# Kernel tuning notes

Hardware: AMD Instinct MI355X
Metric: run time of the kernel (lower is better)

## Reference

```python
import jax, jax.numpy as jnp
import numpy as np

B = 4096
IND = 512
OUTD = 512
DEG = 2
P = 2  # dim_treat
KNOTS = [[0.33, 0.66], [0.33, 0.66]]
D = DEG + 1 + len(KNOTS[0])  # 5 basis functions per treatment dim


def setup_inputs() -> dict:
    key = jax.random.key(0)
    k1, k2, k3 = jax.random.split(key, 3)
    x = jax.random.uniform(k1, (B, P + IND), dtype=jnp.float32)  # treat dims in [0,1]
    weight = jax.random.uniform(k2, (IND, OUTD, D ** P), dtype=jnp.float32)  # torch.rand init
    bias = jax.random.uniform(k3, (OUTD, D ** P), dtype=jnp.float32)
    return {"x": x, "weight": weight, "bias": bias}


def _truncated_power_basis(x_treat):
    # x_treat: [B, P] -> basis: [B, P, D]
    knots = jnp.asarray(KNOTS, dtype=x_treat.dtype)  # [P, n_knots]
    # polynomial part: 1, x, x^2, ... x^DEG
    pows = jnp.stack([x_treat ** i for i in range(DEG + 1)], axis=-1)  # [B, P, DEG+1]
    # truncated part: relu(x - knot)^DEG  (DEG > 1 branch of original code)
    trunc = jax.nn.relu(x_treat[:, :, None] - knots[None, :, :]) ** DEG  # [B, P, n_knots]
    return jnp.concatenate([pows, trunc], axis=-1)


def reference(x, weight, bias):
    x_treat = x[:, :P]          # [B, P]
    x_feature = x[:, P:]        # [B, IND]
    basis = _truncated_power_basis(x_treat)  # [B, P, D]
    # Kronecker product across the two treatment dims: outer product, flattened
    kb = jnp.einsum('bi,bj->bij', basis[:, 0, :], basis[:, 1, :]).reshape(x.shape[0], D * P * 0 + D * D)  # [B, D^2]
    # fused: (weight^T @ x_feature) contracted with the per-sample basis coefficients
    out = jnp.einsum('bi,iod,bd->bo', x_feature, weight, kb)  # [B, OUTD]
    out = out + kb @ bias.T      # bias also varies with treatment basis
    out = jax.nn.relu(out)       # act='relu'
    # islastlayer=0: re-attach treatment dims
    return jnp.concatenate([x_treat, out], axis=1)  # [B, P + OUTD]
```

## Files before the change

### kernel.cpp

```cpp
#include <hip/hip_runtime.h>
#include <hip/hip_bf16.h>
#include <string.h>

#define NB    4096
#define IND_  512
#define OUTD_ 512
#define XCOLS 514
#define ND    25
#define KTOT  12800
#define NSPL  4

#define WT_DS   262144
#define WT_BIAS 6553600

#define BM 32
#define BN 128

#define PWI 64
#define PWO 4
#define PWC (PWO * ND)
#define T8P 112

typedef float  f32x4  __attribute__((ext_vector_type(4)));
typedef int    i32x4  __attribute__((ext_vector_type(4)));
typedef int    i32x8  __attribute__((ext_vector_type(8)));
typedef unsigned short u16x4 __attribute__((ext_vector_type(4)));
typedef unsigned int   u32x2 __attribute__((ext_vector_type(2)));

__device__ __forceinline__ unsigned short f2bf(float f) {
  unsigned int x = __float_as_uint(f);
  return (unsigned short)((x + 0x7fffu + ((x >> 16) & 1u)) >> 16);
}

__device__ __forceinline__ float bf2f(unsigned short u) {
  return __uint_as_float(((unsigned int)u) << 16);
}

__device__ __forceinline__ unsigned int pk_bf16(float a, float b) {
  return (unsigned int)f2bf(a) | ((unsigned int)f2bf(b) << 16);
}

__device__ __forceinline__ unsigned char f2fp8(float v) {
  if (v < 0.015625f) {
    return (unsigned char)__float2int_rn(v * 512.0f);
  }
  unsigned int u = __float_as_uint(v);
  u += 0x7ffffu + ((u >> 20) & 1u);
  int e = (int)(u >> 23) - 127 + 7;
  unsigned int m = (u >> 20) & 7u;
  return (unsigned char)((e << 3) | m);
}

__device__ __forceinline__ float basis_f(float t, int j) {
  switch (j) {
    case 0: return 1.0f;
    case 1: return t;
    case 2: return t * t;
    case 3: { float r = t - 0.33f; r = r > 0.0f ? r : 0.0f; return r * r; }
    default:{ float r = t - 0.66f; r = r > 0.0f ? r : 0.0f; return r * r; }
  }
}

__global__ __launch_bounds__(256) void prep_all_kernel(
    const float* __restrict__ x, const float* __restrict__ W,
    const float* __restrict__ bias, unsigned char* __restrict__ Xf8,
    float* __restrict__ kbDT, unsigned char* __restrict__ kbT8,
    unsigned char* __restrict__ Wt, float* __restrict__ out)
{
  __shared__ unsigned char tile8[PWI * T8P];
  const int bid = blockIdx.x;
  const int tid = threadIdx.x;

  if (bid < 512) {
    const int lane = tid & 63;
    #pragma unroll
    for (int rr = 0; rr < 2; ++rr) {
      const int b = bid * 8 + (tid >> 6) * 2 + rr;
      const float* xr = x + (size_t)b * XCOLS;
      const float* fp = xr + 2 + lane * 8;
      float2 a0 = *(const float2*)(fp + 0);
      float2 a1 = *(const float2*)(fp + 2);
      float2 a2 = *(const float2*)(fp + 4);
      float2 a3 = *(const float2*)(fp + 6);
      float xf[8] = {a0.x, a0.y, a1.x, a1.y, a2.x, a2.y, a3.x, a3.y};
      u32x2 pk;
      pk[0] = (unsigned int)f2fp8(xf[0]) | ((unsigned int)f2fp8(xf[1]) << 8) |
              ((unsigned int)f2fp8(xf[2]) << 16) | ((unsigned int)f2fp8(xf[3]) << 24);
      pk[1] = (unsigned int)f2fp8(xf[4]) | ((unsigned int)f2fp8(xf[5]) << 8) |
              ((unsigned int)f2fp8(xf[6]) << 16) | ((unsigned int)f2fp8(xf[7]) << 24);
      *reinterpret_cast<u32x2*>(Xf8 + (size_t)b * IND_ + lane * 8) = pk;

      float t0 = xr[0], t1 = xr[1];
      if (lane < 2) out[(size_t)b * XCOLS + lane] = (lane == 0) ? t0 : t1;
      {
        int d1 = lane / 5, d2 = lane - d1 * 5;
        float kvd = basis_f(t0, d1) * basis_f(t1, d2);
        float kvn = 0.0f;
        if (lane < 24) {
          int e1 = (lane + 1) / 5, e2 = (lane + 1) - e1 * 5;
          kvn = basis_f(t0, e1) * basis_f(t1, e2);
        }
        if (lane < ND) {
          int bt = b >> 7, bl = b & 15, nf = (b >> 4) & 7;
          kbDT[(((size_t)lane * 32 + bt) * 16 + bl) * 8 + nf] = kvd - kvn;
        }
      }
      {
        int ta = 2 * lane, tb = 2 * lane + 1;
        unsigned char ba = 0, bb = 0;
        if (ta < ND) { int d1 = ta / 5, d2 = ta - d1 * 5;
                       ba = f2fp8(basis_f(t0, d1) * basis_f(t1, d2)); }
        if (tb < ND) { int d1 = tb / 5, d2 = tb - d1 * 5;
                       bb = f2fp8(basis_f(t0, d1) * basis_f(t1, d2)); }
        *(unsigned short*)(kbT8 + (size_t)b * 128 + 2 * lane) =
            (unsigned short)ba | ((unsigned short)bb << 8);
      }
    }
  } else {
    const int pw = bid - 512;
    const int i0 = (pw & 7) * PWI;
    const int o0 = (pw >> 3) * PWO;

    for (int t = tid; t < PWI * (PWC / 4); t += 256) {
      int il = t / (PWC / 4);
      int c4 = t - il * (PWC / 4);
      float4 v = *(const float4*)(W + ((size_t)(i0 + il) * OUTD_ + o0) * ND + c4 * 4);
      unsigned int pk = (unsigned int)f2fp8(v.x) | ((unsigned int)f2fp8(v.y) << 8) |
                        ((unsigned int)f2fp8(v.z) << 16) | ((unsigned int)f2fp8(v.w) << 24);
      *(unsigned int*)&tile8[il * T8P + c4 * 4] = pk;
    }
    __syncthreads();

    for (int g = tid; g < PWC * (PWI / 8); g += 256) {
      int c  = g >> 3;
      int ig = g & 7;
      int d  = c % 25;
      int o_l = c / 25;
      unsigned long long v = 0;
      #pragma unroll
      for (int jj = 0; jj < 8; ++jj)
        v |= (unsigned long long)tile8[(ig * 8 + jj) * T8P + c] << (8 * jj);
      int o  = o0 + o_l;
      int ib = i0 + ig * 8;
      int iw = ib >> 7;
      int wb = ib & 127;
      size_t dest = (((size_t)d * 32 + (o >> 4)) * 4 + iw) * 2048
                  + (size_t)(((wb >> 5) * 16 + (o & 15)) * 32 + (wb & 31));
      *reinterpret_cast<unsigned long long*>(Wt + dest) = v;
    }

    if ((pw & 7) == 0) {
      int o = o0 + (tid >> 6);
      int p = tid & 63;
      int ta = 2 * p, tb = 2 * p + 1;
      unsigned char ba = (ta < ND) ? f2fp8(bias[o * ND + ta]) : (unsigned char)0;
      unsigned char bb = (tb < ND) ? f2fp8(bias[o * ND + tb]) : (unsigned char)0;
      size_t dest = WT_BIAS + (size_t)(o >> 4) * 2048
                  + (size_t)(((ta >> 5) * 16 + (o & 15)) * 32 + (ta & 31));
      *(unsigned short*)(Wt + dest) =
          (unsigned short)ba | ((unsigned short)bb << 8);
    }
  }
}

__global__ __launch_bounds__(256, 3) void gemm_mx_kernel(
    const unsigned char* __restrict__ Wt, const unsigned char* __restrict__ Xf8,
    const float* __restrict__ kbDT, const unsigned char* __restrict__ kbT8,
    unsigned short* __restrict__ Pb)
{
  const int tid  = threadIdx.x;
  const int lane = tid & 63;
  const int w    = tid >> 6;
  const int l15  = lane & 15;
  const int quad = lane >> 4;

  const int id  = blockIdx.x;
  const int ox  = ((id & 7) << 1) | ((id >> 3) & 1);
  const int iw  = (id >> 4) & 3;
  const int by  = id >> 6;

  const int o0 = ox * BM;
  const int b0 = by * BN;
  const bool tail = (iw == 3);

  const int og = ox * 2 + (w >> 1);
  const int bh = w & 1;

  auto load8 = [](const unsigned char* p) -> i32x8 {
    i32x4 lo = *reinterpret_cast<const i32x4*>(p);
    i32x4 hi = *reinterpret_cast<const i32x4*>(p + 16);
    i32x8 v;
    v[0] = lo[0]; v[1] = lo[1]; v[2] = lo[2]; v[3] = lo[3];
    v[4] = hi[0]; v[5] = hi[1]; v[6] = hi[2]; v[7] = hi[3];
    return v;
  };

  i32x8 bfr[4];
  #pragma unroll
  for (int nf = 0; nf < 4; ++nf)
    bfr[nf] = load8(Xf8 + (size_t)(b0 + bh * 64 + nf * 16 + l15) * IND_
                        + iw * 128 + quad * 32);

  const unsigned char* aP =
      Wt + ((size_t)og * 4 + iw) * 2048 + lane * 32;

  const float* dP = kbDT + (((size_t)by * 16 + l15) * 8) + bh * 4;

  f32x4 acc[4], fin[4];
  #pragma unroll
  for (int nf = 0; nf < 4; ++nf) { acc[nf] = (f32x4)0.0f; fin[nf] = (f32x4)0.0f; }

  auto mfma_flush = [&](const i32x8& a, const f32x4& q) {
    #pragma unroll
    for (int nf = 0; nf < 4; ++nf)
      acc[nf] = __builtin_amdgcn_mfma_scale_f32_16x16x128_f8f6f4(
          a, bfr[nf], acc[nf], 0, 0, 0, 0x7f7f7f7f, 0, 0x7f7f7f7f);
    #pragma unroll
    for (int nf = 0; nf < 4; ++nf)
      #pragma unroll
      for (int r = 0; r < 4; ++r)
        fin[nf][r] += q[nf] * acc[nf][r];
  };

  i32x8 a0 = load8(aP);
  i32x8 a1 = load8(aP + WT_DS);
  i32x8 a2;
  f32x4 qA = *reinterpret_cast<const f32x4*>(dP);
  f32x4 qB, qC;

  for (int pass = 0; pass < 8; ++pass) {
    a2 = load8(aP + 2 * WT_DS);
    qB = *reinterpret_cast<const f32x4*>(dP + 4096);
    mfma_flush(a0, qA);

    a0 = load8(aP + 3 * WT_DS);
    qC = *reinterpret_cast<const f32x4*>(dP + 8192);
    mfma_flush(a1, qB);

    a1 = load8(aP + 4 * WT_DS);
    qA = *reinterpret_cast<const f32x4*>(dP + 12288);
    mfma_flush(a2, qC);

    aP += 3 * WT_DS;
    dP += 12288;
  }

  if (tail) a1 = load8(Wt + WT_BIAS + (size_t)og * 2048 + lane * 32);
  mfma_flush(a0, qA);

  if (tail) {
    i32x8 bft[4];
    #pragma unroll
    for (int nf = 0; nf < 4; ++nf)
      bft[nf] = load8(kbT8 + (size_t)(b0 + bh * 64 + nf * 16 + l15) * 128
                           + quad * 32);
    #pragma unroll
    for (int nf = 0; nf < 4; ++nf)
      fin[nf] = __builtin_amdgcn_mfma_scale_f32_16x16x128_f8f6f4(
          a1, bft[nf], fin[nf], 0, 0, 0, 0x7f7f7f7f, 0, 0x7f7f7f7f);
  }

  unsigned short* Pz = Pb + (size_t)iw * NB * OUTD_;
  #pragma unroll
  for (int nf = 0; nf < 4; ++nf) {
    int bg = b0 + bh * 64 + nf * 16 + l15;
    int oo = o0 + (w >> 1) * 16 + quad * 4;
    u32x2 pk;
    pk[0] = pk_bf16(fin[nf][0], fin[nf][1]);
    pk[1] = pk_bf16(fin[nf][2], fin[nf][3]);
    *reinterpret_cast<u32x2*>(&Pz[(size_t)bg * OUTD_ + oo]) = pk;
  }
}

__global__ __launch_bounds__(256) void epilogue_kernel(
    const unsigned short* __restrict__ Pb, float* __restrict__ out)
{
  const int idx = (blockIdx.x * 256 + threadIdx.x) * 4;
  const int b = idx >> 9;
  const int o = idx & 511;
  const size_t ps = (size_t)NB * OUTD_;
  float s[4] = {0.0f, 0.0f, 0.0f, 0.0f};
  #pragma unroll
  for (int z = 0; z < NSPL; ++z) {
    u16x4 v = *reinterpret_cast<const u16x4*>(&Pb[z * ps + idx]);
    #pragma unroll
    for (int e = 0; e < 4; ++e) s[e] += bf2f(v[e]);
  }
  float* op = out + (size_t)b * XCOLS + 2 + o;
  float2 lo, hi;
  lo.x = s[0] > 0.0f ? s[0] : 0.0f;
  lo.y = s[1] > 0.0f ? s[1] : 0.0f;
  hi.x = s[2] > 0.0f ? s[2] : 0.0f;
  hi.y = s[3] > 0.0f ? s[3] : 0.0f;
  *(float2*)op = lo;
  *(float2*)(op + 2) = hi;
}

extern "C" void kernel_launch(void* const* d_in, const int* in_sizes, int n_in,
                              void* d_out, int out_size, void* d_ws, size_t ws_size,
                              hipStream_t stream) {
  const float* x    = (const float*)d_in[0];
  const float* W    = (const float*)d_in[1];
  const float* bias = (const float*)d_in[2];
  float* out = (float*)d_out;
  char* ws = (char*)d_ws;

  const size_t xf_off  = 0;
  const size_t wf_off  = 2097152;
  const size_t kb_off  = wf_off + 6619136;
  const size_t kbt_off = kb_off + 409600;
  const size_t p_off   = kbt_off + (size_t)NB * 128;
  unsigned char* Xf8  = (unsigned char*)(ws + xf_off);
  unsigned char* Wt   = (unsigned char*)(ws + wf_off);
  float* kbDT         = (float*)(ws + kb_off);
  unsigned char* kbT8 = (unsigned char*)(ws + kbt_off);
  unsigned short* Pb  = (unsigned short*)(ws + p_off);

  prep_all_kernel<<<1536, 256, 0, stream>>>(x, W, bias, Xf8, kbDT, kbT8, Wt, out);
  gemm_mx_kernel<<<2048, 256, 0, stream>>>(Wt, Xf8, kbDT, kbT8, Pb);
  epilogue_kernel<<<(NB * OUTD_) / 1024, 256, 0, stream>>>(Pb, out);
}
```

Measured before the change: 129.1 us.

## Remove split-K partials and epilogue; accumulate all K slices in one GEMM kernel

The GEMM kernel now loops over all four input-feature slices inside each block instead of splitting them across blocks. It applies bias and ReLU and writes fp32 output directly, so the bf16 partial buffer and the separate reduction/epilogue kernel are gone. This removes one launch and the partial-sum write/read traffic. In exchange the grid shrinks from 2048 to 512 blocks, which lowers parallelism and occupancy across the CUs and makes each block's serial K loop four times longer.

```diff
diff --git a/kernel.cpp b/kernel.cpp
--- a/kernel.cpp
+++ b/kernel.cpp
@@ -8,7 +8,6 @@
 #define XCOLS 514
 #define ND    25
 #define KTOT  12800
-#define NSPL  4
 
 #define WT_DS   262144
 #define WT_BIAS 6553600
@@ -24,21 +23,7 @@
 typedef float  f32x4  __attribute__((ext_vector_type(4)));
 typedef int    i32x4  __attribute__((ext_vector_type(4)));
 typedef int    i32x8  __attribute__((ext_vector_type(8)));
-typedef unsigned short u16x4 __attribute__((ext_vector_type(4)));
 typedef unsigned int   u32x2 __attribute__((ext_vector_type(2)));
-
-__device__ __forceinline__ unsigned short f2bf(float f) {
-  unsigned int x = __float_as_uint(f);
-  return (unsigned short)((x + 0x7fffu + ((x >> 16) & 1u)) >> 16);
-}
-
-__device__ __forceinline__ float bf2f(unsigned short u) {
-  return __uint_as_float(((unsigned int)u) << 16);
-}
-
-__device__ __forceinline__ unsigned int pk_bf16(float a, float b) {
-  return (unsigned int)f2bf(a) | ((unsigned int)f2bf(b) << 16);
-}
 
 __device__ __forceinline__ unsigned char f2fp8(float v) {
   if (v < 0.015625f) {
@@ -163,10 +148,10 @@
   }
 }
 
-__global__ __launch_bounds__(256, 3) void gemm_mx_kernel(
+__global__ __launch_bounds__(256, 3) void gemm_out_kernel(
     const unsigned char* __restrict__ Wt, const unsigned char* __restrict__ Xf8,
     const float* __restrict__ kbDT, const unsigned char* __restrict__ kbT8,
-    unsigned short* __restrict__ Pb)
+    float* __restrict__ out)
 {
   const int tid  = threadIdx.x;
   const int lane = tid & 63;
@@ -174,14 +159,12 @@
   const int l15  = lane & 15;
   const int quad = lane >> 4;
 
-  const int id  = blockIdx.x;
-  const int ox  = ((id & 7) << 1) | ((id >> 3) & 1);
-  const int iw  = (id >> 4) & 3;
-  const int by  = id >> 6;
+  const int id = blockIdx.x;
+  const int ox = ((id & 7) << 1) | ((id >> 3) & 1);
+  const int by = id >> 4;
 
   const int o0 = ox * BM;
   const int b0 = by * BN;
-  const bool tail = (iw == 3);
 
   const int og = ox * 2 + (w >> 1);
   const int bh = w & 1;
@@ -195,60 +178,66 @@
     return v;
   };
 
-  i32x8 bfr[4];
+  f32x4 fin[4];
   #pragma unroll
-  for (int nf = 0; nf < 4; ++nf)
-    bfr[nf] = load8(Xf8 + (size_t)(b0 + bh * 64 + nf * 16 + l15) * IND_
-                        + iw * 128 + quad * 32);
-
-  const unsigned char* aP =
-      Wt + ((size_t)og * 4 + iw) * 2048 + lane * 32;
-
-  const float* dP = kbDT + (((size_t)by * 16 + l15) * 8) + bh * 4;
-
-  f32x4 acc[4], fin[4];
-  #pragma unroll
-  for (int nf = 0; nf < 4; ++nf) { acc[nf] = (f32x4)0.0f; fin[nf] = (f32x4)0.0f; }
-
-  auto mfma_flush = [&](const i32x8& a, const f32x4& q) {
+  for (int nf = 0; nf < 4; ++nf) fin[nf] = (f32x4)0.0f;
+
+  const float* dBase = kbDT + (((size_t)by * 16 + l15) * 8) + bh * 4;
+
+  for (int iw = 0; iw < 4; ++iw) {
+    i32x8 bfr[4];
     #pragma unroll
     for (int nf = 0; nf < 4; ++nf)
-      acc[nf] = __builtin_amdgcn_mfma_scale_f32_16x16x128_f8f6f4(
-          a, bfr[nf], acc[nf], 0, 0, 0, 0x7f7f7f7f, 0, 0x7f7f7f7f);
-    #pragma unroll
-    for (int nf = 0; nf < 4; ++nf)
+      bfr[nf] = load8(Xf8 + (size_t)(b0 + bh * 64 + nf * 16 + l15) * IND_
+                          + iw * 128 + quad * 32);
+
+    const unsigned char* aP = Wt + ((size_t)og * 4 + iw) * 2048 + lane * 32;
+    const float* dP = dBase;
+
+    f32x4 acc[4];
+    #pragma unroll
+    for (int nf = 0; nf < 4; ++nf) acc[nf] = (f32x4)0.0f;
+
+    auto mfma_flush = [&](const i32x8& a, const f32x4& q) {
       #pragma unroll
-      for (int r = 0; r < 4; ++r)
-        fin[nf][r] += q[nf] * acc[nf][r];
-  };
-
-  i32x8 a0 = load8(aP);
-  i32x8 a1 = load8(aP + WT_DS);
-  i32x8 a2;
-  f32x4 qA = *reinterpret_cast<const f32x4*>(dP);
-  f32x4 qB, qC;
-
-  for (int pass = 0; pass < 8; ++pass) {
-    a2 = load8(aP + 2 * WT_DS);
-    qB = *reinterpret_cast<const f32x4*>(dP + 4096);
+      for (int nf = 0; nf < 4; ++nf)
+        acc[nf] = __builtin_amdgcn_mfma_scale_f32_16x16x128_f8f6f4(
+            a, bfr[nf], acc[nf], 0, 0, 0, 0x7f7f7f7f, 0, 0x7f7f7f7f);
+      #pragma unroll
+      for (int nf = 0; nf < 4; ++nf)
+        #pragma unroll
+        for (int r = 0; r < 4; ++r)
+          fin[nf][r] += q[nf] * acc[nf][r];
+    };
+
+    i32x8 a0 = load8(aP);
+    i32x8 a1 = load8(aP + WT_DS);
+    i32x8 a2;
+    f32x4 qA = *reinterpret_cast<const f32x4*>(dP);
+    f32x4 qB, qC;
+
+    for (int pass = 0; pass < 8; ++pass) {
+      a2 = load8(aP + 2 * WT_DS);
+      qB = *reinterpret_cast<const f32x4*>(dP + 4096);
+      mfma_flush(a0, qA);
+
+      a0 = load8(aP + 3 * WT_DS);
+      qC = *reinterpret_cast<const f32x4*>(dP + 8192);
+      mfma_flush(a1, qB);
+
+      a1 = load8(aP + 4 * WT_DS);
+      qA = *reinterpret_cast<const f32x4*>(dP + 12288);
+      mfma_flush(a2, qC);
+
+      aP += 3 * WT_DS;
+      dP += 12288;
+    }
+
     mfma_flush(a0, qA);
-
-    a0 = load8(aP + 3 * WT_DS);
-    qC = *reinterpret_cast<const f32x4*>(dP + 8192);
-    mfma_flush(a1, qB);
-
-    a1 = load8(aP + 4 * WT_DS);
-    qA = *reinterpret_cast<const f32x4*>(dP + 12288);
-    mfma_flush(a2, qC);
-
-    aP += 3 * WT_DS;
-    dP += 12288;
-  }
-
-  if (tail) a1 = load8(Wt + WT_BIAS + (size_t)og * 2048 + lane * 32);
-  mfma_flush(a0, qA);
-
-  if (tail) {
+  }
+
+  {
+    i32x8 ab = load8(Wt + WT_BIAS + (size_t)og * 2048 + lane * 32);
     i32x8 bft[4];
     #pragma unroll
     for (int nf = 0; nf < 4; ++nf)
@@ -257,43 +246,22 @@
     #pragma unroll
     for (int nf = 0; nf < 4; ++nf)
       fin[nf] = __builtin_amdgcn_mfma_scale_f32_16x16x128_f8f6f4(
-          a1, bft[nf], fin[nf], 0, 0, 0, 0x7f7f7f7f, 0, 0x7f7f7f7f);
-  }
-
-  unsigned short* Pz = Pb + (size_t)iw * NB * OUTD_;
+          ab, bft[nf], fin[nf], 0, 0, 0, 0x7f7f7f7f, 0, 0x7f7f7f7f);
+  }
+
   #pragma unroll
   for (int nf = 0; nf < 4; ++nf) {
     int bg = b0 + bh * 64 + nf * 16 + l15;
     int oo = o0 + (w >> 1) * 16 + quad * 4;
-    u32x2 pk;
-    pk[0] = pk_bf16(fin[nf][0], fin[nf][1]);
-    pk[1] = pk_bf16(fin[nf][2], fin[nf][3]);
-    *reinterpret_cast<u32x2*>(&Pz[(size_t)bg * OUTD_ + oo]) = pk;
-  }
-}
-
-__global__ __launch_bounds__(256) void epilogue_kernel(
-    const unsigned short* __restrict__ Pb, float* __restrict__ out)
-{
-  const int idx = (blockIdx.x * 256 + threadIdx.x) * 4;
-  const int b = idx >> 9;
-  const int o = idx & 511;
-  const size_t ps = (size_t)NB * OUTD_;
-  float s[4] = {0.0f, 0.0f, 0.0f, 0.0f};
-  #pragma unroll
-  for (int z = 0; z < NSPL; ++z) {
-    u16x4 v = *reinterpret_cast<const u16x4*>(&Pb[z * ps + idx]);
-    #pragma unroll
-    for (int e = 0; e < 4; ++e) s[e] += bf2f(v[e]);
-  }
-  float* op = out + (size_t)b * XCOLS + 2 + o;
-  float2 lo, hi;
-  lo.x = s[0] > 0.0f ? s[0] : 0.0f;
-  lo.y = s[1] > 0.0f ? s[1] : 0.0f;
-  hi.x = s[2] > 0.0f ? s[2] : 0.0f;
-  hi.y = s[3] > 0.0f ? s[3] : 0.0f;
-  *(float2*)op = lo;
-  *(float2*)(op + 2) = hi;
+    float* op = out + (size_t)bg * XCOLS + 2 + oo;
+    float2 lo, hi;
+    lo.x = fin[nf][0] > 0.0f ? fin[nf][0] : 0.0f;
+    lo.y = fin[nf][1] > 0.0f ? fin[nf][1] : 0.0f;
+    hi.x = fin[nf][2] > 0.0f ? fin[nf][2] : 0.0f;
+    hi.y = fin[nf][3] > 0.0f ? fin[nf][3] : 0.0f;
+    *(float2*)op = lo;
+    *(float2*)(op + 2) = hi;
+  }
 }
 
 extern "C" void kernel_launch(void* const* d_in, const int* in_sizes, int n_in,
@@ -309,14 +277,11 @@
   const size_t wf_off  = 2097152;
   const size_t kb_off  = wf_off + 6619136;
   const size_t kbt_off = kb_off + 409600;
-  const size_t p_off   = kbt_off + (size_t)NB * 128;
   unsigned char* Xf8  = (unsigned char*)(ws + xf_off);
   unsigned char* Wt   = (unsigned char*)(ws + wf_off);
   float* kbDT         = (float*)(ws + kb_off);
   unsigned char* kbT8 = (unsigned char*)(ws + kbt_off);
-  unsigned short* Pb  = (unsigned short*)(ws + p_off);
 
   prep_all_kernel<<<1536, 256, 0, stream>>>(x, W, bias, Xf8, kbDT, kbT8, Wt, out);
-  gemm_mx_kernel<<<2048, 256, 0, stream>>>(Wt, Xf8, kbDT, kbT8, Pb);
-  epilogue_kernel<<<(NB * OUTD_) / 1024, 256, 0, stream>>>(Pb, out);
-}
+  gemm_out_kernel<<<512, 256, 0, stream>>>(Wt, Xf8, kbDT, kbT8, out);
+}
```

Result: faster. 123.6 us (-4.3%).
